# Performance work log

Measured on AMD Instinct MI355X. Metric: run time of the kernel, lower is better.

The kernel has to match this reference:

```python
import jax, jax.numpy as jnp
import numpy as np

N, R, A, F, T, O = 50000, 5, 8, 128, 2, 128
RADIUS = 1.0

def _template_vertices():
    # polar grid of template vertices in cartesian coords, shape (R, A, 2)
    radii = (np.arange(1, R + 1) / R) * RADIUS
    angles = np.linspace(0.0, 2.0 * np.pi, A, endpoint=False)
    x = radii[:, None] * np.cos(angles)[None, :]
    y = radii[:, None] * np.sin(angles)[None, :]
    return np.stack([x, y], axis=-1)

def _interp_coeffs():
    # Gaussian interpolation coefficients (concrete define_interpolation_coefficients),
    # shape (R, A, R*A), rows normalized -- constant, non-trainable (built in build()).
    v = _template_vertices().reshape(R * A, 2)
    d2 = ((v[:, None, :] - v[None, :, :]) ** 2).sum(-1)
    sigma = RADIUS / R
    w = np.exp(-d2 / (2.0 * sigma ** 2))
    w = w / w.sum(axis=1, keepdims=True)
    return w.reshape(R, A, R * A).astype(np.float32)

def setup_inputs() -> dict:
    key = jax.random.key(0)
    k1, k2, k3, k4, k5 = jax.random.split(key, 5)
    mesh_signal = jax.random.normal(k1, (N, F), dtype=jnp.float32)
    bary_w = jax.random.uniform(k2, (N, R, A, 3), dtype=jnp.float32)
    bary_w = bary_w / bary_w.sum(axis=-1, keepdims=True)  # barycentric weights sum to 1
    bary_idx = jax.random.randint(k3, (N, R, A, 3), 0, N, dtype=jnp.int32)
    glorot = lambda k, shp: jax.random.uniform(
        k, shp, jnp.float32, -1.0, 1.0) * np.sqrt(6.0 / (shp[-1] + shp[-2]))
    template_weights = glorot(k4, (A, T, O, F))  # (n_angular, templates, out, feat)
    bias = glorot(k5, (T, O))
    return {"mesh_signal": mesh_signal, "bary_w": bary_w,
            "template_weights": template_weights, "bias": bias,
            "interp_coeffs": jnp.asarray(_interp_coeffs()),
            "bary_idx": bary_idx}

def reference(mesh_signal, bary_w, template_weights, bias, interp_coeffs, bary_idx):
    # --- patch operator: barycentric gather + interpolation ---
    gathered = mesh_signal[bary_idx]                       # (N,R,A,3,F) irregular gather
    interp = (bary_w[..., None] * gathered).sum(axis=-2)   # (N,R,A,F)
    # prior: mix all R*A template-vertex signals per output template vertex
    sig = interp.reshape(-1, R * A, F)                     # (N,RA,F)
    interp = jnp.einsum('nkf,rak->nraf', sig, interp_coeffs)  # (N,R,A,F)
    # --- fold: all A rotations (rotation_delta=1), vectorized by rolling weights ---
    rots = jnp.arange(0, A, 1)                             # K = A rotations
    idx = (jnp.arange(A)[None, :] + rots[:, None]) % A     # (K,A): roll(interp,+r) == roll(W,-r)
    W_all = template_weights[idx]                          # (K,A,T,O,F)
    # TF adds bias before summing over (R,A) axes -> bias appears R*A times
    z = jnp.einsum('nraf,katof->nkto', interp, W_all) + (R * A) * bias  # (N,K,T,O)
    out = jax.nn.relu(z).sum(axis=2)                       # sum over templates -> (N,K,O)
    return out
```

## Files before the change

kernel.cpp:

```cpp
#include <hip/hip_runtime.h>
#include <hip/hip_bf16.h>
#include <stdint.h>

#define NN 50000
#define RR 5
#define AA 8
#define FF 128
#define TT 2
#define OO 128
#define KDIM 1024
#define NCOLS 2048
#define RA 40

typedef __attribute__((ext_vector_type(8))) short short8;
typedef __attribute__((ext_vector_type(4))) float f32x4;
typedef __attribute__((ext_vector_type(4))) int i32x4;

__device__ inline void gload_lds16(const void* g, void* l) {
  __builtin_amdgcn_global_load_lds(
      (const __attribute__((address_space(1))) unsigned int*)g,
      (__attribute__((address_space(3))) unsigned int*)l, 16, 0, 0);
}

__global__ void prep_kernel(const float* __restrict__ mesh,
                            const float* __restrict__ coeffs,
                            const float* __restrict__ W,
                            __hip_bfloat16* __restrict__ meshq,
                            float* __restrict__ C2,
                            __hip_bfloat16* __restrict__ BmatT) {
  int tid = blockIdx.x * blockDim.x + threadIdx.x;
  int stride = gridDim.x * blockDim.x;
  for (int i = tid; i < NN * FF; i += stride) {
    int n = i >> 7, f = i & 127;
    int p = f >> 5, fo = f & 31;
    meshq[((long)p * NN + n) * 32 + fo] = __float2bfloat16(mesh[i]);
  }
  for (int i = tid; i < AA * RA; i += stride) {
    int a = i / RA, k = i % RA;
    float s = 0.f;
    for (int r = 0; r < RR; ++r) s += coeffs[(r * AA + a) * RA + k];
    C2[i] = s;
  }
  for (int i = tid; i < NCOLS * KDIM; i += stride) {
    int c = i >> 10, kf = i & 1023;
    int kr = c >> 8, t = (c >> 7) & 1, o = c & 127;
    int a = kf >> 7, f = kf & 127;
    int arot = (a + kr) & 7;
    BmatT[i] = __float2bfloat16(W[((arot * TT + t) * OO + o) * FF + f]);
  }
}

__global__ __launch_bounds__(256) void s_pass_kernel(
    const __hip_bfloat16* __restrict__ meshq,
    const float* __restrict__ bary_w,
    const int* __restrict__ bary_idx,
    const float* __restrict__ C2,
    __hip_bfloat16* __restrict__ Sout,
    int p) {
  __shared__ float w_s[16 * 120];
  __shared__ int i_s[16 * 120];
  __shared__ float c2_s[AA * RA];
  int tid = threadIdx.x;
  long n0 = (long)blockIdx.x * 16;

  const f32x4* wsrc = (const f32x4*)(bary_w + n0 * 120);
  const i32x4* isrc = (const i32x4*)(bary_idx + n0 * 120);
  for (int i = tid; i < 480; i += 256) {
    f32x4 wv = __builtin_nontemporal_load(wsrc + i);
    ((f32x4*)w_s)[i] = wv;
    i32x4 iv = __builtin_nontemporal_load(isrc + i);
    ((i32x4*)i_s)[i] = iv;
  }
  for (int i = tid; i < AA * RA; i += 256) c2_s[i] = C2[i];
  __syncthreads();

  int g = tid >> 4;
  int fo = tid & 15;
  long n = n0 + g;
  const float* wg = w_s + g * 120;
  const int* ig = i_s + g * 120;
  const char* mbase = (const char*)(meshq + (long)p * NN * 32) + fo * 4;

  float sx_acc[AA], sy_acc[AA];
#pragma unroll
  for (int a = 0; a < AA; ++a) { sx_acc[a] = 0.f; sy_acc[a] = 0.f; }

#pragma unroll 2
  for (int k = 0; k < RA; ++k) {
    float sx = 0.f, sy = 0.f;
#pragma unroll
    for (int j = 0; j < 3; ++j) {
      int row = ig[k * 3 + j];
      unsigned u = *(const unsigned*)(mbase + (long)row * 64);
      float w = wg[k * 3 + j];
      sx += w * __uint_as_float(u << 16);
      sy += w * __uint_as_float(u & 0xffff0000u);
    }
#pragma unroll
    for (int a = 0; a < AA; ++a) {
      float c = c2_s[a * RA + k];
      sx_acc[a] += c * sx;
      sy_acc[a] += c * sy;
    }
  }

  long base = n * KDIM + p * 32 + fo * 2;
#pragma unroll
  for (int a = 0; a < AA; ++a) {
    __hip_bfloat16 hx = __float2bfloat16(sx_acc[a]);
    __hip_bfloat16 hy = __float2bfloat16(sy_acc[a]);
    unsigned u = (unsigned)*(unsigned short*)&hx | ((unsigned)*(unsigned short*)&hy << 16);
    __builtin_nontemporal_store(u, (unsigned*)(Sout + base + a * FF));
  }
}

__global__ __launch_bounds__(512) void gemm_kernel(
    const __hip_bfloat16* __restrict__ S,
    const __hip_bfloat16* __restrict__ BT,
    const float* __restrict__ bias,
    float* __restrict__ out) {
  int kr = blockIdx.x;
  int mt = blockIdx.y;
  int row0 = mt * 128;
  int col0 = kr * 256;
  int tid = threadIdx.x;
  int lane = tid & 63;
  int wid = tid >> 6;
  int wave_m = wid >> 2;
  int wave_n = wid & 3;

  __shared__ __align__(16) char lds[49152];

  f32x4 acc[4][4];
#pragma unroll
  for (int m = 0; m < 4; ++m)
#pragma unroll
    for (int q = 0; q < 4; ++q) acc[m][q] = (f32x4){0.f, 0.f, 0.f, 0.f};

  for (int kt = 0; kt < KDIM / 64; ++kt) {
    int k0 = kt * 64;
#pragma unroll
    for (int i = 0; i < 2; ++i) {
      int li = i * 512 + tid;
      int r = li >> 3, s = li & 7;
      int sp = s ^ (r & 7);
      int row = row0 + r;
      if (row >= NN) row = NN - 1;
      gload_lds16(S + (long)row * KDIM + k0 + sp * 8, lds + li * 16);
    }
#pragma unroll
    for (int i = 0; i < 4; ++i) {
      int li = i * 512 + tid;
      int r = li >> 3, s = li & 7;
      int sp = s ^ (r & 7);
      gload_lds16(BT + (long)(col0 + r) * KDIM + k0 + sp * 8, lds + 16384 + li * 16);
    }
    __syncthreads();
#pragma unroll
    for (int kk = 0; kk < 2; ++kk) {
      short8 afr[4], bfr[4];
#pragma unroll
      for (int m = 0; m < 4; ++m) {
        int arow = wave_m * 64 + m * 16 + (lane & 15);
        int slot = (kk * 4 + (lane >> 4)) ^ (arow & 7);
        afr[m] = *(const short8*)(lds + arow * 128 + slot * 16);
      }
#pragma unroll
      for (int q = 0; q < 4; ++q) {
        int bcol = (q >> 1) * 128 + wave_n * 32 + (q & 1) * 16 + (lane & 15);
        int slot = (kk * 4 + (lane >> 4)) ^ (bcol & 7);
        bfr[q] = *(const short8*)(lds + 16384 + bcol * 128 + slot * 16);
      }
#pragma unroll
      for (int m = 0; m < 4; ++m)
#pragma unroll
        for (int q = 0; q < 4; ++q)
          acc[m][q] = __builtin_amdgcn_mfma_f32_16x16x32_bf16(afr[m], bfr[q], acc[m][q], 0, 0, 0);
    }
    __syncthreads();
  }

  int olo = wave_n * 32 + (lane & 15);
  float b00 = 40.f * bias[olo];
  float b01 = 40.f * bias[olo + 16];
  float b10 = 40.f * bias[OO + olo];
  float b11 = 40.f * bias[OO + olo + 16];
#pragma unroll
  for (int m = 0; m < 4; ++m) {
#pragma unroll
    for (int i = 0; i < 4; ++i) {
      int node = row0 + wave_m * 64 + m * 16 + (lane >> 4) * 4 + i;
      if (node < NN) {
        float r0 = fmaxf(acc[m][0][i] + b00, 0.f) + fmaxf(acc[m][2][i] + b10, 0.f);
        float r1 = fmaxf(acc[m][1][i] + b01, 0.f) + fmaxf(acc[m][3][i] + b11, 0.f);
        long base = (long)node * 1024 + kr * 128;
        out[base + olo] = r0;
        out[base + olo + 16] = r1;
      }
    }
  }
}

extern "C" void kernel_launch(void* const* d_in, const int* in_sizes, int n_in,
                              void* d_out, int out_size, void* d_ws, size_t ws_size,
                              hipStream_t stream) {
  const float* mesh   = (const float*)d_in[0];
  const float* bary_w = (const float*)d_in[1];
  const float* W      = (const float*)d_in[2];
  const float* bias   = (const float*)d_in[3];
  const float* coeffs = (const float*)d_in[4];
  const int* bidx     = (const int*)d_in[5];
  float* out = (float*)d_out;
  char* ws = (char*)d_ws;

  __hip_bfloat16* meshq = (__hip_bfloat16*)ws;
  float* C2             = (float*)(ws + 12800000);
  __hip_bfloat16* BmatT = (__hip_bfloat16*)(ws + 12801280);
  __hip_bfloat16* Smat  = (__hip_bfloat16*)(ws + 16995584);

  prep_kernel<<<dim3(2048), dim3(256), 0, stream>>>(mesh, coeffs, W, meshq, C2, BmatT);
  for (int p = 0; p < 4; ++p)
    s_pass_kernel<<<dim3(3125), dim3(256), 0, stream>>>(meshq, bary_w, bidx, C2, Smat, p);
  gemm_kernel<<<dim3(8, 391), dim3(512), 0, stream>>>(Smat, BmatT, bias, out);
}
```

Measured before the change: 449.6 us.

## Pack bary weights/indices to 32-bit and triple-buffer a larger GEMM tile

Prep now packs each barycentric index (upper 16 bits) and bf16 weight (lower 16 bits) into one 32-bit word, so each of the four gather passes reads half the metadata bytes. The GEMM grows its M tile to 256 rows with 8x4 MFMA accumulators per wave, uses a triple-buffered LDS pipeline with K-step 32 and explicit vmcnt waits, remaps blocks for L2 locality, and writes output with nontemporal stores. Storing the index in 16 bits overflows because indices reach 50000 (above 32767 is fine unsigned, but above 65535 is not). The unsigned shift does hold 50000, though bf16 weights lose precision. Packing only runs when the workspace is large enough, and the 1-block-per-CU GEMM risks lower occupancy.

```diff
diff --git a/kernel.cpp b/kernel.cpp
--- a/kernel.cpp
+++ b/kernel.cpp
@@ -11,6 +11,7 @@
 #define KDIM 1024
 #define NCOLS 2048
 #define RA 40
+#define NT 32
 
 typedef __attribute__((ext_vector_type(8))) short short8;
 typedef __attribute__((ext_vector_type(4))) float f32x4;
@@ -25,9 +26,13 @@
 __global__ void prep_kernel(const float* __restrict__ mesh,
                             const float* __restrict__ coeffs,
                             const float* __restrict__ W,
+                            const float* __restrict__ bary_w,
+                            const int* __restrict__ bary_idx,
                             __hip_bfloat16* __restrict__ meshq,
                             float* __restrict__ C2,
-                            __hip_bfloat16* __restrict__ BmatT) {
+                            __hip_bfloat16* __restrict__ BmatT,
+                            unsigned* __restrict__ packb,
+                            int do_pack) {
   int tid = blockIdx.x * blockDim.x + threadIdx.x;
   int stride = gridDim.x * blockDim.x;
   for (int i = tid; i < NN * FF; i += stride) {
@@ -47,6 +52,71 @@
     int a = kf >> 7, f = kf & 127;
     int arot = (a + kr) & 7;
     BmatT[i] = __float2bfloat16(W[((arot * TT + t) * OO + o) * FF + f]);
+  }
+  if (do_pack) {
+    for (int i = tid; i < NN * 120; i += stride) {
+      __hip_bfloat16 h = __float2bfloat16(bary_w[i]);
+      unsigned wb = *(unsigned short*)&h;
+      packb[i] = ((unsigned)bary_idx[i] << 16) | wb;
+    }
+  }
+}
+
+__global__ __launch_bounds__(256) void s_pass_packed(
+    const __hip_bfloat16* __restrict__ meshq,
+    const unsigned* __restrict__ packb,
+    const float* __restrict__ C2,
+    __hip_bfloat16* __restrict__ Sout,
+    int p) {
+  __shared__ unsigned pk_s[16 * 120];
+  __shared__ float c2_s[AA * RA];
+  int tid = threadIdx.x;
+  long n0 = (long)blockIdx.x * 16;
+  const i32x4* psrc = (const i32x4*)(packb + n0 * 120);
+  for (int i = tid; i < 480; i += 256) {
+    i32x4 v = __builtin_nontemporal_load(psrc + i);
+    ((i32x4*)pk_s)[i] = v;
+  }
+  for (int i = tid; i < AA * RA; i += 256) c2_s[i] = C2[i];
+  __syncthreads();
+
+  int g = tid >> 4;
+  int fo = tid & 15;
+  long n = n0 + g;
+  const unsigned* pg = pk_s + g * 120;
+  const char* mbase = (const char*)(meshq + (long)p * NN * 32) + fo * 4;
+
+  float sx_acc[AA], sy_acc[AA];
+#pragma unroll
+  for (int a = 0; a < AA; ++a) { sx_acc[a] = 0.f; sy_acc[a] = 0.f; }
+
+#pragma unroll 2
+  for (int k = 0; k < RA; ++k) {
+    float sx = 0.f, sy = 0.f;
+#pragma unroll
+    for (int j = 0; j < 3; ++j) {
+      unsigned v = pg[k * 3 + j];
+      unsigned row = v >> 16;
+      float w = __uint_as_float(v << 16);
+      unsigned u = *(const unsigned*)(mbase + (long)row * 64);
+      sx += w * __uint_as_float(u << 16);
+      sy += w * __uint_as_float(u & 0xffff0000u);
+    }
+#pragma unroll
+    for (int a = 0; a < AA; ++a) {
+      float c = c2_s[a * RA + k];
+      sx_acc[a] += c * sx;
+      sy_acc[a] += c * sy;
+    }
+  }
+
+  long base = n * KDIM + p * 32 + fo * 2;
+#pragma unroll
+  for (int a = 0; a < AA; ++a) {
+    __hip_bfloat16 hx = __float2bfloat16(sx_acc[a]);
+    __hip_bfloat16 hy = __float2bfloat16(sy_acc[a]);
+    unsigned u = (unsigned)*(unsigned short*)&hx | ((unsigned)*(unsigned short*)&hy << 16);
+    __builtin_nontemporal_store(u, (unsigned*)(Sout + base + a * FF));
   }
 }
 
@@ -62,7 +132,6 @@
   __shared__ float c2_s[AA * RA];
   int tid = threadIdx.x;
   long n0 = (long)blockIdx.x * 16;
-
   const f32x4* wsrc = (const f32x4*)(bary_w + n0 * 120);
   const i32x4* isrc = (const i32x4*)(bary_idx + n0 * 120);
   for (int i = tid; i < 480; i += 256) {
@@ -73,18 +142,15 @@
   }
   for (int i = tid; i < AA * RA; i += 256) c2_s[i] = C2[i];
   __syncthreads();
-
   int g = tid >> 4;
   int fo = tid & 15;
   long n = n0 + g;
   const float* wg = w_s + g * 120;
   const int* ig = i_s + g * 120;
   const char* mbase = (const char*)(meshq + (long)p * NN * 32) + fo * 4;
-
   float sx_acc[AA], sy_acc[AA];
 #pragma unroll
   for (int a = 0; a < AA; ++a) { sx_acc[a] = 0.f; sy_acc[a] = 0.f; }
-
 #pragma unroll 2
   for (int k = 0; k < RA; ++k) {
     float sx = 0.f, sy = 0.f;
@@ -103,7 +169,6 @@
       sy_acc[a] += c * sy;
     }
   }
-
   long base = n * KDIM + p * 32 + fo * 2;
 #pragma unroll
   for (int a = 0; a < AA; ++a) {
@@ -114,70 +179,94 @@
   }
 }
 
-__global__ __launch_bounds__(512) void gemm_kernel(
+__global__ __launch_bounds__(512, 1) void gemm_kernel(
     const __hip_bfloat16* __restrict__ S,
     const __hip_bfloat16* __restrict__ BT,
     const float* __restrict__ bias,
     float* __restrict__ out) {
-  int kr = blockIdx.x;
-  int mt = blockIdx.y;
-  int row0 = mt * 128;
+  int bx = blockIdx.x;
+  int by = blockIdx.y;
+  int kr = by & 7;
+  int mt = ((by >> 3) << 3) + bx;
+  if (mt >= 196) return;
+  int row0 = mt * 256;
   int col0 = kr * 256;
+
   int tid = threadIdx.x;
   int lane = tid & 63;
   int wid = tid >> 6;
   int wave_m = wid >> 2;
   int wave_n = wid & 3;
 
-  __shared__ __align__(16) char lds[49152];
-
-  f32x4 acc[4][4];
-#pragma unroll
-  for (int m = 0; m < 4; ++m)
+  __shared__ __align__(16) char lds[98304];
+
+  f32x4 acc[8][4];
+#pragma unroll
+  for (int m = 0; m < 8; ++m)
 #pragma unroll
     for (int q = 0; q < 4; ++q) acc[m][q] = (f32x4){0.f, 0.f, 0.f, 0.f};
 
-  for (int kt = 0; kt < KDIM / 64; ++kt) {
-    int k0 = kt * 64;
-#pragma unroll
-    for (int i = 0; i < 2; ++i) {
-      int li = i * 512 + tid;
-      int r = li >> 3, s = li & 7;
-      int sp = s ^ (r & 7);
-      int row = row0 + r;
-      if (row >= NN) row = NN - 1;
-      gload_lds16(S + (long)row * KDIM + k0 + sp * 8, lds + li * 16);
-    }
-#pragma unroll
-    for (int i = 0; i < 4; ++i) {
-      int li = i * 512 + tid;
-      int r = li >> 3, s = li & 7;
-      int sp = s ^ (r & 7);
-      gload_lds16(BT + (long)(col0 + r) * KDIM + k0 + sp * 8, lds + 16384 + li * 16);
-    }
-    __syncthreads();
-#pragma unroll
-    for (int kk = 0; kk < 2; ++kk) {
-      short8 afr[4], bfr[4];
-#pragma unroll
-      for (int m = 0; m < 4; ++m) {
-        int arow = wave_m * 64 + m * 16 + (lane & 15);
-        int slot = (kk * 4 + (lane >> 4)) ^ (arow & 7);
-        afr[m] = *(const short8*)(lds + arow * 128 + slot * 16);
-      }
-#pragma unroll
-      for (int q = 0; q < 4; ++q) {
-        int bcol = (q >> 1) * 128 + wave_n * 32 + (q & 1) * 16 + (lane & 15);
-        int slot = (kk * 4 + (lane >> 4)) ^ (bcol & 7);
-        bfr[q] = *(const short8*)(lds + 16384 + bcol * 128 + slot * 16);
-      }
-#pragma unroll
-      for (int m = 0; m < 4; ++m)
-#pragma unroll
-        for (int q = 0; q < 4; ++q)
-          acc[m][q] = __builtin_amdgcn_mfma_f32_16x16x32_bf16(afr[m], bfr[q], acc[m][q], 0, 0, 0);
-    }
-    __syncthreads();
+#define STAGE(T, B)                                                         \
+  {                                                                         \
+    int k0_ = (T) * 32;                                                     \
+    char* base_ = lds + (B) * 32768;                                        \
+    _Pragma("unroll")                                                       \
+    for (int i_ = 0; i_ < 2; ++i_) {                                        \
+      int li_ = i_ * 512 + tid;                                             \
+      int r_ = li_ >> 2, sp_ = li_ & 3;                                     \
+      int sl_ = sp_ ^ ((r_ >> 1) & 3);                                      \
+      int row_ = row0 + r_;                                                 \
+      if (row_ >= NN) row_ = NN - 1;                                        \
+      gload_lds16(S + (long)row_ * KDIM + k0_ + sl_ * 8, base_ + li_ * 16); \
+    }                                                                       \
+    _Pragma("unroll")                                                       \
+    for (int i_ = 0; i_ < 2; ++i_) {                                        \
+      int li_ = i_ * 512 + tid;                                             \
+      int r_ = li_ >> 2, sp_ = li_ & 3;                                     \
+      int sl_ = sp_ ^ ((r_ >> 1) & 3);                                      \
+      gload_lds16(BT + (long)(col0 + r_) * KDIM + k0_ + sl_ * 8,            \
+                  base_ + 16384 + li_ * 16);                                \
+    }                                                                       \
+  }
+
+  STAGE(0, 0)
+  STAGE(1, 1)
+
+  int bcur = 0, bstage = 2;
+  for (int t = 0; t < NT; ++t) {
+    if (t < NT - 1) {
+      asm volatile("s_waitcnt vmcnt(4)" ::: "memory");
+    } else {
+      asm volatile("s_waitcnt vmcnt(0)" ::: "memory");
+    }
+    __builtin_amdgcn_sched_barrier(0);
+    __builtin_amdgcn_s_barrier();
+    __builtin_amdgcn_sched_barrier(0);
+    if (t + 2 < NT) STAGE(t + 2, bstage)
+    const char* base = lds + bcur * 32768;
+    short8 afr[8], bfr[4];
+#pragma unroll
+    for (int m = 0; m < 8; ++m) {
+      int r = wave_m * 128 + m * 16 + (lane & 15);
+      int phys = (lane >> 4) ^ ((r >> 1) & 3);
+      afr[m] = *(const short8*)(base + r * 64 + phys * 16);
+    }
+#pragma unroll
+    for (int q = 0; q < 4; ++q) {
+      int c = (q >> 1) * 128 + wave_n * 32 + (q & 1) * 16 + (lane & 15);
+      int phys = (lane >> 4) ^ ((c >> 1) & 3);
+      bfr[q] = *(const short8*)(base + 16384 + c * 64 + phys * 16);
+    }
+    __builtin_amdgcn_s_setprio(1);
+#pragma unroll
+    for (int m = 0; m < 8; ++m)
+#pragma unroll
+      for (int q = 0; q < 4; ++q)
+        acc[m][q] = __builtin_amdgcn_mfma_f32_16x16x32_bf16(afr[m], bfr[q], acc[m][q], 0, 0, 0);
+    __builtin_amdgcn_s_setprio(0);
+    __builtin_amdgcn_sched_barrier(0);
+    bcur = (bcur == 2) ? 0 : bcur + 1;
+    bstage = (bstage == 2) ? 0 : bstage + 1;
   }
 
   int olo = wave_n * 32 + (lane & 15);
@@ -186,16 +275,16 @@
   float b10 = 40.f * bias[OO + olo];
   float b11 = 40.f * bias[OO + olo + 16];
 #pragma unroll
-  for (int m = 0; m < 4; ++m) {
+  for (int m = 0; m < 8; ++m) {
 #pragma unroll
     for (int i = 0; i < 4; ++i) {
-      int node = row0 + wave_m * 64 + m * 16 + (lane >> 4) * 4 + i;
+      int node = row0 + wave_m * 128 + m * 16 + (lane >> 4) * 4 + i;
       if (node < NN) {
         float r0 = fmaxf(acc[m][0][i] + b00, 0.f) + fmaxf(acc[m][2][i] + b10, 0.f);
         float r1 = fmaxf(acc[m][1][i] + b01, 0.f) + fmaxf(acc[m][3][i] + b11, 0.f);
         long base = (long)node * 1024 + kr * 128;
-        out[base + olo] = r0;
-        out[base + olo + 16] = r1;
+        __builtin_nontemporal_store(r0, out + base + olo);
+        __builtin_nontemporal_store(r1, out + base + olo + 16);
       }
     }
   }
@@ -217,9 +306,18 @@
   float* C2             = (float*)(ws + 12800000);
   __hip_bfloat16* BmatT = (__hip_bfloat16*)(ws + 12801280);
   __hip_bfloat16* Smat  = (__hip_bfloat16*)(ws + 16995584);
-
-  prep_kernel<<<dim3(2048), dim3(256), 0, stream>>>(mesh, coeffs, W, meshq, C2, BmatT);
-  for (int p = 0; p < 4; ++p)
-    s_pass_kernel<<<dim3(3125), dim3(256), 0, stream>>>(meshq, bary_w, bidx, C2, Smat, p);
-  gemm_kernel<<<dim3(8, 391), dim3(512), 0, stream>>>(Smat, BmatT, bias, out);
-}
+  unsigned* packb       = (unsigned*)(ws + 119395584);
+
+  int do_pack = (ws_size >= 143395584UL) ? 1 : 0;
+
+  prep_kernel<<<dim3(2048), dim3(256), 0, stream>>>(mesh, coeffs, W, bary_w, bidx,
+                                                    meshq, C2, BmatT, packb, do_pack);
+  if (do_pack) {
+    for (int p = 0; p < 4; ++p)
+      s_pass_packed<<<dim3(3125), dim3(256), 0, stream>>>(meshq, packb, C2, Smat, p);
+  } else {
+    for (int p = 0; p < 4; ++p)
+      s_pass_kernel<<<dim3(3125), dim3(256), 0, stream>>>(meshq, bary_w, bidx, C2, Smat, p);
+  }
+  gemm_kernel<<<dim3(8, 200), dim3(512), 0, stream>>>(Smat, BmatT, bias, out);
+}
```

New measurement: 426.6 us. 1.05x faster.
